# Performance work log

Hardware: AMD Instinct MI355X
Metric: run time of the kernel (lower is better)

Reference implementation:

```python
import jax, jax.numpy as jnp
import numpy as np

NEG_INF = -1e9  # matches masked_fill value -1000000000.0
SLOPE = 0.2     # LeakyReLU negative slope


def setup_inputs() -> dict:
    key = jax.random.key(0)
    k1, k2, k3, k4 = jax.random.split(key, 4)
    B, N, Fin, Fout = 16, 1024, 256, 256
    h = jax.random.normal(k1, (B, N, Fin), dtype=jnp.float32)
    adj = jax.random.randint(k2, (B, N, N), 0, 2, dtype=jnp.int32)
    W = jax.random.normal(k3, (Fin, Fout), dtype=jnp.float32) * (1.0 / np.sqrt(Fin))
    a = jax.random.normal(k4, (2 * Fout,), dtype=jnp.float32) * (1.0 / np.sqrt(2 * Fout))
    return {"h": h, "adj": adj, "W": W, "a": a}


def reference(h, adj, W, a):
    # h: [B,N,Fin], adj: [B,N,N] (0/1), W: [Fin,Fout], a: [2*Fout]
    Fout = W.shape[1]
    Wh = jnp.einsum("bnf,fo->bno", h, W)            # [B,N,Fout]
    a1, a2 = a[:Fout], a[Fout:]
    # e[b,i,j] = leakyrelu( Wh[b,i]·a1 + Wh[b,j]·a2 )  == a(cat(Wh_i, Wh_j))
    f1 = Wh @ a1                                     # [B,N]
    f2 = Wh @ a2                                     # [B,N]
    e = jax.nn.leaky_relu(f1[:, :, None] + f2[:, None, :], negative_slope=SLOPE)
    e = jnp.where(adj == 0, NEG_INF, e)              # mask non-edges
    attention = jax.nn.softmax(e, axis=-1)           # [B,N,N]
    # dropout is identity at eval / p=0
    h_prime = jnp.einsum("bij,bjo->bio", attention, Wh)  # [B,N,Fout]
    return h_prime
```

## Files before the change

kernel.cpp:

```cpp
#include <hip/hip_runtime.h>

typedef __attribute__((ext_vector_type(8))) short bf16x8;
typedef __attribute__((ext_vector_type(4))) float f32x4;

__device__ __forceinline__ unsigned short f2bf(float x) {
    unsigned int u = __float_as_uint(x);
    u += 0x7FFFu + ((u >> 16) & 1u);
    return (unsigned short)(u >> 16);
}

__device__ __forceinline__ void gl_lds16(const void* g, void* l) {
    __builtin_amdgcn_global_load_lds(
        (__attribute__((address_space(1))) void*)((void*)g),
        (__attribute__((address_space(3))) void*)l, 16, 0, 0);
}

#define SFENCE __builtin_amdgcn_sched_barrier(0)

__global__ __launch_bounds__(256) void prep(const float* __restrict__ W,
                                            short* __restrict__ WbT) {
    __shared__ float tile[32][33];
    const int t = threadIdx.x;
    const int bx = blockIdx.x & 7, by = blockIdx.x >> 3;
    const int r0 = by * 32, c0 = bx * 32;
    const int lr = t >> 5, lc = t & 31;
#pragma unroll
    for (int q = 0; q < 4; ++q)
        tile[q * 8 + lr][lc] = W[(r0 + q * 8 + lr) * 256 + c0 + lc];
    __syncthreads();
#pragma unroll
    for (int q = 0; q < 4; ++q)
        WbT[(c0 + q * 8 + lr) * 256 + r0 + lc] = (short)f2bf(tile[lc][q * 8 + lr]);
}

__global__ __launch_bounds__(256, 4) void setup2(const float* __restrict__ h,
                                                 const short* __restrict__ WbT,
                                                 const float* __restrict__ a,
                                                 const int* __restrict__ adj,
                                                 short* __restrict__ WhT,
                                                 float* __restrict__ f1,
                                                 float* __restrict__ f2,
                                                 unsigned long long* __restrict__ bits) {
    __shared__ short hA[32][264];
    __shared__ float sp[2][4][32];
    const int t = threadIdx.x;
    const int wid = t >> 6, lane = t & 63;

    if (blockIdx.x >= 512) {
        const int row = (blockIdx.x - 512) * 4 + wid;
        const int* arow = adj + (size_t)row * 1024;
        unsigned long long myword = 0ull;
#pragma unroll
        for (int w = 0; w < 16; ++w) {
            int v = arow[w * 64 + lane];
            unsigned long long bal = __ballot(v != 0);
            if (lane == w) myword = bal;
        }
        if (lane < 16) bits[(size_t)row * 16 + lane] = myword;
        return;
    }

    const int quad = lane >> 4, l15 = lane & 15;
    const int m0 = blockIdx.x * 32;

#pragma unroll
    for (int rr = 0; rr < 2; ++rr) {
        const int r = rr * 16 + (t >> 4), c0 = (t & 15) * 16;
        const float* hp = h + (size_t)(m0 + r) * 256 + c0;
        float4 v0 = *(const float4*)(hp + 0), v1 = *(const float4*)(hp + 4);
        float4 v2 = *(const float4*)(hp + 8), v3 = *(const float4*)(hp + 12);
        bf16x8 w0, w1;
        w0[0] = (short)f2bf(v0.x); w0[1] = (short)f2bf(v0.y);
        w0[2] = (short)f2bf(v0.z); w0[3] = (short)f2bf(v0.w);
        w0[4] = (short)f2bf(v1.x); w0[5] = (short)f2bf(v1.y);
        w0[6] = (short)f2bf(v1.z); w0[7] = (short)f2bf(v1.w);
        w1[0] = (short)f2bf(v2.x); w1[1] = (short)f2bf(v2.y);
        w1[2] = (short)f2bf(v2.z); w1[3] = (short)f2bf(v2.w);
        w1[4] = (short)f2bf(v3.x); w1[5] = (short)f2bf(v3.y);
        w1[6] = (short)f2bf(v3.z); w1[7] = (short)f2bf(v3.w);
        *(bf16x8*)&hA[r][c0] = w0;
        *(bf16x8*)&hA[r][c0 + 8] = w1;
    }
    __syncthreads();

    f32x4 acc[2][4] = {};
#pragma unroll
    for (int kt = 0; kt < 8; ++kt) {
        const int k0 = kt * 32;
        bf16x8 bv[4];
#pragma unroll
        for (int ft = 0; ft < 4; ++ft)
            bv[ft] = *(const bf16x8*)(WbT + (size_t)(wid * 64 + ft * 16 + l15) * 256 + k0 + quad * 8);
        bf16x8 a0 = *(const bf16x8*)&hA[l15][k0 + quad * 8];
        bf16x8 a1 = *(const bf16x8*)&hA[16 + l15][k0 + quad * 8];
#pragma unroll
        for (int ft = 0; ft < 4; ++ft) {
            acc[0][ft] = __builtin_amdgcn_mfma_f32_16x16x32_bf16(a0, bv[ft], acc[0][ft], 0, 0, 0);
            acc[1][ft] = __builtin_amdgcn_mfma_f32_16x16x32_bf16(a1, bv[ft], acc[1][ft], 0, 0, 0);
        }
    }

    const int b = m0 >> 10;
#pragma unroll
    for (int mf = 0; mf < 2; ++mf) {
        const int il0 = (m0 & 1023) + mf * 16 + quad * 4;
#pragma unroll
        for (int ft = 0; ft < 4; ++ft) {
            const int f = wid * 64 + ft * 16 + l15;
            ushort4 pk;
            pk.x = f2bf(acc[mf][ft][0]);
            pk.y = f2bf(acc[mf][ft][1]);
            pk.z = f2bf(acc[mf][ft][2]);
            pk.w = f2bf(acc[mf][ft][3]);
            *(ushort4*)(WhT + ((size_t)b << 18) + (size_t)f * 1024 + il0) = pk;
        }
    }

    float a1v[4], a2v[4];
#pragma unroll
    for (int ft = 0; ft < 4; ++ft) {
        a1v[ft] = a[wid * 64 + ft * 16 + l15];
        a2v[ft] = a[256 + wid * 64 + ft * 16 + l15];
    }
    float p1[2][4] = {}, p2[2][4] = {};
#pragma unroll
    for (int mf = 0; mf < 2; ++mf)
#pragma unroll
        for (int ft = 0; ft < 4; ++ft)
#pragma unroll
            for (int r = 0; r < 4; ++r) {
                p1[mf][r] += acc[mf][ft][r] * a1v[ft];
                p2[mf][r] += acc[mf][ft][r] * a2v[ft];
            }
#pragma unroll
    for (int off = 1; off < 16; off <<= 1)
#pragma unroll
        for (int mf = 0; mf < 2; ++mf)
#pragma unroll
            for (int r = 0; r < 4; ++r) {
                p1[mf][r] += __shfl_xor(p1[mf][r], off);
                p2[mf][r] += __shfl_xor(p2[mf][r], off);
            }
    if (l15 == 0)
#pragma unroll
        for (int mf = 0; mf < 2; ++mf)
#pragma unroll
            for (int r = 0; r < 4; ++r) {
                sp[0][wid][mf * 16 + quad * 4 + r] = p1[mf][r];
                sp[1][wid][mf * 16 + quad * 4 + r] = p2[mf][r];
            }
    __syncthreads();
    if (t < 32) {
        f1[m0 + t] = sp[0][0][t] + sp[0][1][t] + sp[0][2][t] + sp[0][3][t];
        f2[m0 + t] = sp[1][0][t] + sp[1][1][t] + sp[1][2][t] + sp[1][3][t];
    }
}

__global__ __launch_bounds__(512, 2) void fused_agg(const unsigned long long* __restrict__ bitsG,
                                                    const float* __restrict__ f1g,
                                                    const float* __restrict__ f2g,
                                                    const short* __restrict__ WhT,
                                                    float* __restrict__ out) {
    __shared__ short Bs[3][256 * 64];
    __shared__ short Ps[2][64 * 64];
    __shared__ unsigned long long bitsS[16 * 64];
    __shared__ float f2s[1024];
    __shared__ float lred[512];
    __shared__ float linv[64];

    const int t = threadIdx.x;
    const int wid = t >> 6, lane = t & 63;
    const int quad = lane >> 4, l15 = lane & 15;

    const int id = blockIdx.x;
    const int xcd = id & 7, rest = id >> 3;
    const int b = xcd + 8 * (rest & 1);
    const int m0 = (rest >> 1) * 64;

    const short* Wb = WhT + ((size_t)b << 18);

    {
        const unsigned long long* bsrc = bitsG + (size_t)((b << 10) + m0) * 16;
        ulonglong2 bv = ((const ulonglong2*)bsrc)[t];
        const int g0 = 2 * t, g1 = 2 * t + 1;
        bitsS[(g0 & 15) * 64 + (g0 >> 4)] = bv.x;
        bitsS[(g1 & 15) * 64 + (g1 >> 4)] = bv.y;
        ((float2*)f2s)[t] = ((const float2*)(f2g + (b << 10)))[t];
    }
    const int pr = t >> 3, ps = t & 7;
    const float f1r = f1g[(b << 10) + m0 + pr];
    __syncthreads();

    auto stage = [&](int T, short* buf) {
#pragma unroll
        for (int q = 0; q < 4; ++q) {
            const int c = t + 512 * q;
            const int rr = c >> 3;
            const int sl = (c & 7) ^ (rr & 7);
            gl_lds16(Wb + (size_t)rr * 1024 + T * 64 + sl * 8, buf + c * 8);
        }
    };

    float lacc = 0.f;
    auto pgen = [&](int T, short* pbuf) {
        unsigned int m8 = (unsigned int)(bitsS[T * 64 + pr] >> (ps * 8)) & 0xffu;
        float4 fa = *(const float4*)(f2s + T * 64 + ps * 8);
        float4 fb = *(const float4*)(f2s + T * 64 + ps * 8 + 4);
        float xv[8] = {fa.x, fa.y, fa.z, fa.w, fb.x, fb.y, fb.z, fb.w};
        bf16x8 pw;
#pragma unroll
        for (int u = 0; u < 8; ++u) {
            float x = f1r + xv[u];
            x = fmaxf(x, 0.2f * x);
            float pv = ((m8 >> u) & 1u) ? __expf(x) : 0.f;
            lacc += pv;
            pw[u] = (short)f2bf(pv);
        }
        *(bf16x8*)(pbuf + pr * 64 + ((ps ^ (pr & 7)) * 8)) = pw;
    };

    const int wm = wid >> 2, wn = wid & 3;
    const int mh = wm * 32, nq = wn * 64;
    f32x4 acc[2][4] = {};

    auto step = [&](const short* pbuf, const short* bbuf) {
#pragma unroll
        for (int kt = 0; kt < 2; ++kt) {
            const int w = kt * 4 + quad;
            bf16x8 av[2], bv[4];
#pragma unroll
            for (int mf = 0; mf < 2; ++mf) {
                const int ra = mh + mf * 16 + l15;
                av[mf] = *(const bf16x8*)(pbuf + ra * 64 + ((w ^ (ra & 7)) * 8));
            }
#pragma unroll
            for (int nf = 0; nf < 4; ++nf) {
                const int rb = nq + nf * 16 + l15;
                bv[nf] = *(const bf16x8*)(bbuf + rb * 64 + ((w ^ (rb & 7)) * 8));
            }
#pragma unroll
            for (int mf = 0; mf < 2; ++mf)
#pragma unroll
                for (int nf = 0; nf < 4; ++nf)
                    acc[mf][nf] = __builtin_amdgcn_mfma_f32_16x16x32_bf16(av[mf], bv[nf], acc[mf][nf], 0, 0, 0);
        }
    };

    stage(0, Bs[0]);
    stage(1, Bs[1]);
    pgen(0, Ps[0]);
    asm volatile("s_waitcnt lgkmcnt(0)" ::: "memory");
    SFENCE;
    asm volatile("s_waitcnt vmcnt(4)" ::: "memory");
    SFENCE;
    __builtin_amdgcn_s_barrier();
    SFENCE;

#pragma unroll
    for (int T = 0; T < 16; ++T) {
        if (T < 14) stage(T + 2, Bs[(T + 2) % 3]);
        if (T < 15) pgen(T + 1, Ps[(T + 1) & 1]);
        __builtin_amdgcn_s_setprio(1);
        step(Ps[T & 1], Bs[T % 3]);
        __builtin_amdgcn_s_setprio(0);
        asm volatile("s_waitcnt lgkmcnt(0)" ::: "memory");
        SFENCE;
        if (T < 14) {
            asm volatile("s_waitcnt vmcnt(4)" ::: "memory");
        } else if (T == 14) {
            asm volatile("s_waitcnt vmcnt(0)" ::: "memory");
        }
        SFENCE;
        __builtin_amdgcn_s_barrier();
        SFENCE;
    }

    lred[t] = lacc;
    __syncthreads();
    if (t < 64) {
        const float* lp = lred + t * 8;
        linv[t] = 1.0f / (((lp[0] + lp[1]) + (lp[2] + lp[3])) +
                          ((lp[4] + lp[5]) + (lp[6] + lp[7])));
    }
    __syncthreads();

#pragma unroll
    for (int mf = 0; mf < 2; ++mf) {
        const int il = mh + mf * 16 + quad * 4;
        const float i0 = linv[il], i1 = linv[il + 1];
        const float i2 = linv[il + 2], i3 = linv[il + 3];
#pragma unroll
        for (int nf = 0; nf < 4; ++nf) {
            float* op = out + (size_t)((b << 10) + m0 + il) * 256 + nq + nf * 16 + l15;
            op[0]   = acc[mf][nf][0] * i0;
            op[256] = acc[mf][nf][1] * i1;
            op[512] = acc[mf][nf][2] * i2;
            op[768] = acc[mf][nf][3] * i3;
        }
    }
}

extern "C" void kernel_launch(void* const* d_in, const int* in_sizes, int n_in,
                              void* d_out, int out_size, void* d_ws, size_t ws_size,
                              hipStream_t stream) {
    const float* h   = (const float*)d_in[0];
    const int*   adj = (const int*)d_in[1];
    const float* W   = (const float*)d_in[2];
    const float* a   = (const float*)d_in[3];
    float* out = (float*)d_out;

    short* WbT = (short*)d_ws;
    float* f1  = (float*)(WbT + 65536);
    float* f2  = f1 + 16384;
    short* WhT = (short*)(f2 + 16384);
    unsigned long long* bits =
        (unsigned long long*)(WhT + 16 * 256 * 1024);

    prep<<<64, 256, 0, stream>>>(W, WbT);
    setup2<<<4608, 256, 0, stream>>>(h, WbT, a, adj, WhT, f1, f2, bits);
    fused_agg<<<256, 512, 0, stream>>>(bits, f1, f2, WhT, out);
}
```

Before: 137.2 us.

## Split fused aggregation across output-column halves to double grid size

Each fused_agg block now computes only 128 of the 256 output columns, so the grid doubles to 512 blocks. The staged B tiles and per-wave accumulators shrink by half, and the softmax reduction scratch now reuses the P buffer, which cuts LDS use and allows higher occupancy (launch bounds raised to 4). The cost is that the P generation (exp and masking) is duplicated across the two column-half blocks. Separately, the adjacency and h loads in setup2 now use nontemporal loads to avoid polluting the cache.

```diff
diff --git a/kernel.cpp b/kernel.cpp
--- a/kernel.cpp
+++ b/kernel.cpp
@@ -2,6 +2,8 @@
 
 typedef __attribute__((ext_vector_type(8))) short bf16x8;
 typedef __attribute__((ext_vector_type(4))) float f32x4;
+typedef __attribute__((ext_vector_type(4))) float fvec4;
+typedef __attribute__((ext_vector_type(4))) int ivec4;
 
 __device__ __forceinline__ unsigned short f2bf(float x) {
     unsigned int u = __float_as_uint(x);
@@ -52,7 +54,7 @@
         unsigned long long myword = 0ull;
 #pragma unroll
         for (int w = 0; w < 16; ++w) {
-            int v = arow[w * 64 + lane];
+            int v = __builtin_nontemporal_load(arow + w * 64 + lane);
             unsigned long long bal = __ballot(v != 0);
             if (lane == w) myword = bal;
         }
@@ -67,17 +69,18 @@
     for (int rr = 0; rr < 2; ++rr) {
         const int r = rr * 16 + (t >> 4), c0 = (t & 15) * 16;
         const float* hp = h + (size_t)(m0 + r) * 256 + c0;
-        float4 v0 = *(const float4*)(hp + 0), v1 = *(const float4*)(hp + 4);
-        float4 v2 = *(const float4*)(hp + 8), v3 = *(const float4*)(hp + 12);
+        fvec4 v0 = __builtin_nontemporal_load((const fvec4*)(hp + 0));
+        fvec4 v1 = __builtin_nontemporal_load((const fvec4*)(hp + 4));
+        fvec4 v2 = __builtin_nontemporal_load((const fvec4*)(hp + 8));
+        fvec4 v3 = __builtin_nontemporal_load((const fvec4*)(hp + 12));
         bf16x8 w0, w1;
-        w0[0] = (short)f2bf(v0.x); w0[1] = (short)f2bf(v0.y);
-        w0[2] = (short)f2bf(v0.z); w0[3] = (short)f2bf(v0.w);
-        w0[4] = (short)f2bf(v1.x); w0[5] = (short)f2bf(v1.y);
-        w0[6] = (short)f2bf(v1.z); w0[7] = (short)f2bf(v1.w);
-        w1[0] = (short)f2bf(v2.x); w1[1] = (short)f2bf(v2.y);
-        w1[2] = (short)f2bf(v2.z); w1[3] = (short)f2bf(v2.w);
-        w1[4] = (short)f2bf(v3.x); w1[5] = (short)f2bf(v3.y);
-        w1[6] = (short)f2bf(v3.z); w1[7] = (short)f2bf(v3.w);
+#pragma unroll
+        for (int u = 0; u < 4; ++u) {
+            w0[u]     = (short)f2bf(v0[u]);
+            w0[u + 4] = (short)f2bf(v1[u]);
+            w1[u]     = (short)f2bf(v2[u]);
+            w1[u + 4] = (short)f2bf(v3[u]);
+        }
         *(bf16x8*)&hA[r][c0] = w0;
         *(bf16x8*)&hA[r][c0 + 8] = w1;
     }
@@ -156,17 +159,15 @@
     }
 }
 
-__global__ __launch_bounds__(512, 2) void fused_agg(const unsigned long long* __restrict__ bitsG,
+__global__ __launch_bounds__(512, 4) void fused_agg(const unsigned long long* __restrict__ bitsG,
                                                     const float* __restrict__ f1g,
                                                     const float* __restrict__ f2g,
                                                     const short* __restrict__ WhT,
                                                     float* __restrict__ out) {
-    __shared__ short Bs[3][256 * 64];
-    __shared__ short Ps[2][64 * 64];
+    __shared__ __align__(16) short Bs[3][128 * 64];
+    __shared__ __align__(16) short Ps[2][64 * 64];
     __shared__ unsigned long long bitsS[16 * 64];
     __shared__ float f2s[1024];
-    __shared__ float lred[512];
-    __shared__ float linv[64];
 
     const int t = threadIdx.x;
     const int wid = t >> 6, lane = t & 63;
@@ -175,7 +176,9 @@
     const int id = blockIdx.x;
     const int xcd = id & 7, rest = id >> 3;
     const int b = xcd + 8 * (rest & 1);
-    const int m0 = (rest >> 1) * 64;
+    const int r2 = rest >> 1;
+    const int n0 = (r2 & 1) * 128;
+    const int m0 = (r2 >> 1) * 64;
 
     const short* Wb = WhT + ((size_t)b << 18);
 
@@ -193,11 +196,11 @@
 
     auto stage = [&](int T, short* buf) {
 #pragma unroll
-        for (int q = 0; q < 4; ++q) {
+        for (int q = 0; q < 2; ++q) {
             const int c = t + 512 * q;
             const int rr = c >> 3;
             const int sl = (c & 7) ^ (rr & 7);
-            gl_lds16(Wb + (size_t)rr * 1024 + T * 64 + sl * 8, buf + c * 8);
+            gl_lds16(Wb + (size_t)(n0 + rr) * 1024 + T * 64 + sl * 8, buf + c * 8);
         }
     };
 
@@ -220,28 +223,28 @@
     };
 
     const int wm = wid >> 2, wn = wid & 3;
-    const int mh = wm * 32, nq = wn * 64;
-    f32x4 acc[2][4] = {};
+    const int mh = wm * 32, nq = wn * 32;
+    f32x4 acc[2][2] = {};
 
     auto step = [&](const short* pbuf, const short* bbuf) {
 #pragma unroll
         for (int kt = 0; kt < 2; ++kt) {
             const int w = kt * 4 + quad;
-            bf16x8 av[2], bv[4];
+            bf16x8 av[2], bv[2];
 #pragma unroll
             for (int mf = 0; mf < 2; ++mf) {
                 const int ra = mh + mf * 16 + l15;
                 av[mf] = *(const bf16x8*)(pbuf + ra * 64 + ((w ^ (ra & 7)) * 8));
             }
 #pragma unroll
-            for (int nf = 0; nf < 4; ++nf) {
+            for (int nf = 0; nf < 2; ++nf) {
                 const int rb = nq + nf * 16 + l15;
                 bv[nf] = *(const bf16x8*)(bbuf + rb * 64 + ((w ^ (rb & 7)) * 8));
             }
 #pragma unroll
             for (int mf = 0; mf < 2; ++mf)
 #pragma unroll
-                for (int nf = 0; nf < 4; ++nf)
+                for (int nf = 0; nf < 2; ++nf)
                     acc[mf][nf] = __builtin_amdgcn_mfma_f32_16x16x32_bf16(av[mf], bv[nf], acc[mf][nf], 0, 0, 0);
         }
     };
@@ -251,7 +254,7 @@
     pgen(0, Ps[0]);
     asm volatile("s_waitcnt lgkmcnt(0)" ::: "memory");
     SFENCE;
-    asm volatile("s_waitcnt vmcnt(4)" ::: "memory");
+    asm volatile("s_waitcnt vmcnt(2)" ::: "memory");
     SFENCE;
     __builtin_amdgcn_s_barrier();
     SFENCE;
@@ -266,7 +269,7 @@
         asm volatile("s_waitcnt lgkmcnt(0)" ::: "memory");
         SFENCE;
         if (T < 14) {
-            asm volatile("s_waitcnt vmcnt(4)" ::: "memory");
+            asm volatile("s_waitcnt vmcnt(2)" ::: "memory");
         } else if (T == 14) {
             asm volatile("s_waitcnt vmcnt(0)" ::: "memory");
         }
@@ -275,6 +278,8 @@
         SFENCE;
     }
 
+    float* lred = (float*)&Ps[0][0];
+    float* linv = lred + 512;
     lred[t] = lacc;
     __syncthreads();
     if (t < 64) {
@@ -290,8 +295,8 @@
         const float i0 = linv[il], i1 = linv[il + 1];
         const float i2 = linv[il + 2], i3 = linv[il + 3];
 #pragma unroll
-        for (int nf = 0; nf < 4; ++nf) {
-            float* op = out + (size_t)((b << 10) + m0 + il) * 256 + nq + nf * 16 + l15;
+        for (int nf = 0; nf < 2; ++nf) {
+            float* op = out + (size_t)((b << 10) + m0 + il) * 256 + n0 + nq + nf * 16 + l15;
             op[0]   = acc[mf][nf][0] * i0;
             op[256] = acc[mf][nf][1] * i1;
             op[512] = acc[mf][nf][2] * i2;
@@ -318,5 +323,5 @@
 
     prep<<<64, 256, 0, stream>>>(W, WbT);
     setup2<<<4608, 256, 0, stream>>>(h, WbT, a, adj, WhT, f1, f2, bits);
-    fused_agg<<<256, 512, 0, stream>>>(bits, f1, f2, WhT, out);
-}
+    fused_agg<<<512, 512, 0, stream>>>(bits, f1, f2, WhT, out);
+}
```

New measurement: 145.1 us. 5.8% more time.
